# Kernel optimization log

Hardware: AMD Instinct MI355X
Metric: run time of the kernel (lower is better)

## Reference

```python
import jax, jax.numpy as jnp
import numpy as np
import math

D_MODEL = 2048
NUM_HEADS = 32
NUM_KV_HEADS = 8
HEAD_DIM = D_MODEL // NUM_HEADS  # 64
BATCH = 2
SEQ = 2048


def setup_inputs() -> dict:
    key = jax.random.key(0)
    ks = jax.random.split(key, 5)
    std_q = math.sqrt(2.0 / (D_MODEL + D_MODEL))
    std_kv = math.sqrt(2.0 / (D_MODEL + NUM_KV_HEADS * HEAD_DIM))
    x = jax.random.normal(ks[0], (BATCH, SEQ, D_MODEL), dtype=jnp.float32)
    Wq = jax.random.normal(ks[1], (D_MODEL, D_MODEL), dtype=jnp.float32) * std_q
    Wk = jax.random.normal(ks[2], (NUM_KV_HEADS * HEAD_DIM, D_MODEL), dtype=jnp.float32) * std_kv
    Wv = jax.random.normal(ks[3], (NUM_KV_HEADS * HEAD_DIM, D_MODEL), dtype=jnp.float32) * std_kv
    Wo = jax.random.normal(ks[4], (D_MODEL, D_MODEL), dtype=jnp.float32) * std_q
    return {"x": x, "Wq": Wq, "Wk": Wk, "Wv": Wv, "Wo": Wo}


def reference(x, Wq, Wk, Wv, Wo):
    B, L, _ = x.shape
    group = NUM_HEADS // NUM_KV_HEADS
    # projections: x @ W.T
    q = (x @ Wq.T).reshape(B, L, NUM_HEADS, HEAD_DIM).transpose(0, 2, 1, 3)      # [B,H,L,D]
    k = (x @ Wk.T).reshape(B, L, NUM_KV_HEADS, HEAD_DIM).transpose(0, 2, 1, 3)   # [B,Hkv,L,D]
    v = (x @ Wv.T).reshape(B, L, NUM_KV_HEADS, HEAD_DIM).transpose(0, 2, 1, 3)
    # expand KV heads (repeat_interleave along head dim)
    k = jnp.repeat(k, group, axis=1)  # [B,H,L,D]
    v = jnp.repeat(v, group, axis=1)
    scale = 1.0 / math.sqrt(HEAD_DIM)
    scores = jnp.einsum("bhld,bhsd->bhls", q, k) * scale  # [B,H,L,S]
    causal_mask = jnp.tril(jnp.ones((L, L), dtype=bool))
    scores = jnp.where(causal_mask[None, None], scores, -jnp.inf)
    weights = jax.nn.softmax(scores, axis=-1)
    out = jnp.einsum("bhls,bhsd->bhld", weights, v)  # [B,H,L,D]
    out = out.transpose(0, 2, 1, 3).reshape(B, L, D_MODEL)
    return out @ Wo.T
```

## Files before the change

### kernel.cpp

```cpp
#include <hip/hip_runtime.h>
#include <stdint.h>


typedef unsigned short u16;
typedef short bf16x8 __attribute__((ext_vector_type(8)));
typedef float f32x4 __attribute__((ext_vector_type(4)));

#define D_MODEL 2048
#define QKV_DIM 3072
#define NUM_HEADS 32
#define HEAD_DIM 64
#define SEQ 2048
#define MTOT 4096

static __device__ __forceinline__ u16 f2bf(float f){
  uint32_t u = __builtin_bit_cast(uint32_t, f);
  u += 0x7FFFu + ((u >> 16) & 1u);
  return (u16)(u >> 16);
}

static __device__ __forceinline__ float exp2_fast(float x){
  float r;
  asm("v_exp_f32 %0, %1" : "=v"(r) : "v"(x));
  return r;
}

static __device__ __forceinline__ uint32_t cvt_pk_bf16(float lo, float hi){
  uint32_t r;
  asm("v_cvt_pk_bf16_f32 %0, %1, %2" : "=v"(r) : "v"(lo), "v"(hi));
  return r;
}

static __device__ __forceinline__ void gload16(const u16* g, u16* l){
  __builtin_amdgcn_global_load_lds(
      (__attribute__((address_space(1))) uint32_t*)(uintptr_t)g,
      (__attribute__((address_space(3))) uint32_t*)l,
      16, 0, 0);
}

static __device__ __forceinline__ void cvt8(const float* __restrict__ src,
                                            u16* __restrict__ dst,
                                            int i, float scl){
  float4 a = *(const float4*)(src + i);
  float4 b = *(const float4*)(src + i + 4);
  union { u16 h[8]; uint4 v; } t;
  t.h[0]=f2bf(a.x*scl); t.h[1]=f2bf(a.y*scl); t.h[2]=f2bf(a.z*scl); t.h[3]=f2bf(a.w*scl);
  t.h[4]=f2bf(b.x*scl); t.h[5]=f2bf(b.y*scl); t.h[6]=f2bf(b.z*scl); t.h[7]=f2bf(b.w*scl);
  *(uint4*)(dst + i) = t.v;
}

__global__ __launch_bounds__(256)
void cvt_bf16(const float* __restrict__ in, u16* __restrict__ out, int n,
              float scl){
  const int i = (blockIdx.x * 256 + threadIdx.x) * 8;
  if (i >= n) return;
  cvt8(in, out, i, scl);
}

__global__ __launch_bounds__(256)
void cvt_all(const float* __restrict__ x,  const float* __restrict__ Wq,
             const float* __restrict__ Wk, const float* __restrict__ Wv,
             const float* __restrict__ Wo,
             u16* __restrict__ xb, u16* __restrict__ Wb,
             u16* __restrict__ Wob, float qscl){
  const int bid = blockIdx.x;
  const float* src; u16* dst; int off; float scl = 1.0f;
  if (bid < 4096){        src = x;  dst = xb;                              off = bid;        }
  else if (bid < 6144){   src = Wq; dst = Wb;                              off = bid - 4096; scl = qscl; }
  else if (bid < 6656){   src = Wk; dst = Wb + (size_t)D_MODEL*D_MODEL;    off = bid - 6144; }
  else if (bid < 7168){   src = Wv; dst = Wb + (size_t)2560*D_MODEL;       off = bid - 6656; }
  else {                  src = Wo; dst = Wob;                             off = bid - 7168; }
  const int i = (off * 256 + threadIdx.x) * 8;
  cvt8(src, dst, i, scl);
}

template <bool F32OUT>
__global__ __launch_bounds__(256)
void gemm_bt(const u16* __restrict__ A, const u16* __restrict__ B,
             void* __restrict__ Cv, int M, int N, int K, int nbx){
  constexpr int BK = 32;
  __shared__ __attribute__((aligned(16))) u16 As[128*BK];
  __shared__ __attribute__((aligned(16))) u16 Bs[128*BK];
  const int tid  = threadIdx.x;
  const int wave = tid >> 6, lane = tid & 63;
  const int quad = lane >> 4, l16 = lane & 15;
  const int wrow = wave >> 1, wcol = wave & 1;
  const int nwg = gridDim.x;
  const int qq = nwg >> 3, rr = nwg & 7;
  const int xcd = blockIdx.x & 7, lin = blockIdx.x >> 3;
  const int swz = (xcd < rr ? xcd*(qq+1) : rr*(qq+1) + (xcd-rr)*qq) + lin;
  const int m0 = (swz / nbx) * 128, n0 = (swz % nbx) * 128;
  const int srow = lane >> 2, scol = (lane & 3) * 8;

  const f32x4 zero = {0.f, 0.f, 0.f, 0.f};
  f32x4 acc[4][4];
#pragma unroll
  for (int i = 0; i < 4; i++)
#pragma unroll
    for (int j = 0; j < 4; j++) acc[i][j] = zero;

  for (int k0 = 0; k0 < K; k0 += BK){
#pragma unroll
    for (int t = 0; t < 2; t++){
      const int chunk = wave + t*4;
      gload16(A + (size_t)(m0 + chunk*16 + srow)*K + k0 + scol, As + chunk*16*BK);
      gload16(B + (size_t)(n0 + chunk*16 + srow)*K + k0 + scol, Bs + chunk*16*BK);
    }
    __syncthreads();
    bf16x8 af[4], bfr[4];
#pragma unroll
    for (int mi = 0; mi < 4; mi++)
      af[mi] = *(const bf16x8*)(As + (wrow*64 + mi*16 + l16)*BK + quad*8);
#pragma unroll
    for (int ni = 0; ni < 4; ni++)
      bfr[ni] = *(const bf16x8*)(Bs + (wcol*64 + ni*16 + l16)*BK + quad*8);
#pragma unroll
    for (int mi = 0; mi < 4; mi++)
#pragma unroll
      for (int ni = 0; ni < 4; ni++)
        acc[mi][ni] = __builtin_amdgcn_mfma_f32_16x16x32_bf16(af[mi], bfr[ni], acc[mi][ni], 0, 0, 0);
    __syncthreads();
  }
#pragma unroll
  for (int mi = 0; mi < 4; mi++)
#pragma unroll
    for (int ni = 0; ni < 4; ni++){
      const int col = n0 + wcol*64 + ni*16 + l16;
#pragma unroll
      for (int r = 0; r < 4; r++){
        const int row = m0 + wrow*64 + mi*16 + quad*4 + r;
        if constexpr (F32OUT)
          ((float*)Cv)[(size_t)row*N + col] = acc[mi][ni][r];
        else
          ((u16*)Cv)[(size_t)row*N + col] = f2bf(acc[mi][ni][r]);
      }
    }
}

__global__ __launch_bounds__(256)
void kvtrans(const u16* __restrict__ QKV, u16* __restrict__ Ksw,
             u16* __restrict__ Vsw){
  __shared__ u16 Ls[64*72];
  const int tid = threadIdx.x;
  const int st = blockIdx.x, hk = blockIdx.y, b = blockIdx.z;
  const size_t rb = (size_t)b * SEQ;
  const size_t tbase = ((size_t)(b*8 + hk)*32 + st) * 4096;

#pragma unroll
  for (int t = 0; t < 2; t++){
    const int task = t*256 + tid;
    const int r = task >> 3, c = task & 7;
    uint4 kv = *(const uint4*)(QKV + (rb + st*64 + r)*QKV_DIM + 2048 + hk*HEAD_DIM + c*8);
    *(uint4*)(Ksw + tbase + r*64 + (size_t)((c ^ (r & 7)) * 8)) = kv;
  }
#pragma unroll
  for (int t = 0; t < 2; t++){
    const int task = t*256 + tid;
    const int r = task >> 3, c = task & 7;
    *(uint4*)(Ls + r*72 + c*8) =
        *(const uint4*)(QKV + (rb + st*64 + r)*QKV_DIM + 2560 + hk*HEAD_DIM + c*8);
  }
  __syncthreads();
#pragma unroll
  for (int t = 0; t < 2; t++){
    const int task = t*256 + tid;
    const int d = task >> 3, sc = task & 7;
    union { u16 h[8]; uint4 v; } tmp;
#pragma unroll
    for (int e = 0; e < 8; e++){
      const int key = ((2*(sc>>2) + (e>>2))<<4) + ((sc&3)<<2) + (e&3);
      tmp.h[e] = Ls[key*72 + d];
    }
    *(uint4*)(Vsw + tbase + d*64 + (size_t)((sc ^ (d & 7)) * 8)) = tmp.v;
  }
}

__global__ __launch_bounds__(256)
void attn(const u16* __restrict__ Q, const u16* __restrict__ Ksw,
          const u16* __restrict__ Vsw, u16* __restrict__ O, int qs){
  __shared__ __attribute__((aligned(16))) u16 Ks[2][64*64];
  __shared__ __attribute__((aligned(16))) u16 Vt[2][64*64];
  const int tid = threadIdx.x;
  const int wave = tid >> 6, lane = tid & 63, quad = lane >> 4, l16 = lane & 15;
  const int g_ = (blockIdx.x + blockIdx.y) & 31;
  const int qt = blockIdx.z ? (31 - g_) : g_;
  const int h = blockIdx.y, b = blockIdx.z;
  const int hk = h >> 2;
  const size_t rb = (size_t)b * SEQ;
  const size_t hb = ((size_t)(b*8 + hk)) * 32;

  const int qrow = wave*16 + l16;
  const int sw = l16 & 7;

  bf16x8 qf[2];
  {
    const u16* qp = Q + (rb + qt*64 + wave*16 + l16)*qs + h*HEAD_DIM;
    qf[0] = *(const bf16x8*)(qp + quad*8);
    qf[1] = *(const bf16x8*)(qp + 32 + quad*8);
  }
  const f32x4 zero = {0.f, 0.f, 0.f, 0.f};
  f32x4 oacc[4];
#pragma unroll
  for (int i = 0; i < 4; i++) oacc[i] = zero;
  float m_i = -INFINITY;
  float l_i = 0.f;

  {
    const u16* kt = Ksw + hb * 4096;
    const u16* vt = Vsw + hb * 4096;
#pragma unroll
    for (int t = 0; t < 2; t++){
      const int ch = wave*2 + t;
      gload16(kt + ch*512 + lane*8, &Ks[0][ch*512]);
      gload16(vt + ch*512 + lane*8, &Vt[0][ch*512]);
    }
  }
  int cur = 0;

  for (int j = 0; j <= qt; ++j){
    __syncthreads();
    if (j < qt){
      const u16* kt = Ksw + (hb + j + 1) * 4096;
      const u16* vt = Vsw + (hb + j + 1) * 4096;
#pragma unroll
      for (int t = 0; t < 2; t++){
        const int ch = wave*2 + t;
        gload16(kt + ch*512 + lane*8, &Ks[cur^1][ch*512]);
        gload16(vt + ch*512 + lane*8, &Vt[cur^1][ch*512]);
      }
    }
    const u16* Ksb = Ks[cur];
    const u16* Vtb = Vt[cur];

    f32x4 st[4];
#pragma unroll
    for (int ni = 0; ni < 4; ni++){
      f32x4 s = zero;
#pragma unroll
      for (int ss = 0; ss < 2; ss++){
        bf16x8 kf = *(const bf16x8*)(Ksb + ((ni*16 + l16) << 6) +
                                     (((ss*4 + quad) ^ sw) << 3));
        s = __builtin_amdgcn_mfma_f32_16x16x32_bf16(kf, qf[ss], s, 0, 0, 0);
      }
      st[ni] = s;
    }
    if (j == qt){
#pragma unroll
      for (int ni = 0; ni < 4; ni++)
#pragma unroll
        for (int r = 0; r < 4; r++)
          if (ni*16 + quad*4 + r > qrow) st[ni][r] = -INFINITY;
    }

    float mx = fmaxf(fmaxf(fmaxf(st[0][0], st[0][1]), fmaxf(st[0][2], st[0][3])),
                     fmaxf(fmaxf(st[1][0], st[1][1]), fmaxf(st[1][2], st[1][3])));
    mx = fmaxf(mx, fmaxf(fmaxf(fmaxf(st[2][0], st[2][1]), fmaxf(st[2][2], st[2][3])),
                         fmaxf(fmaxf(st[3][0], st[3][1]), fmaxf(st[3][2], st[3][3]))));
    mx = fmaxf(mx, __shfl_xor(mx, 16));
    mx = fmaxf(mx, __shfl_xor(mx, 32));

    if (__all(mx <= m_i + 10.f)){
      float ps = 0.f;
#pragma unroll
      for (int ni = 0; ni < 4; ni++)
#pragma unroll
        for (int r = 0; r < 4; r++){
          const float p = exp2_fast(st[ni][r] - m_i);
          st[ni][r] = p;
          ps += p;
        }
      ps += __shfl_xor(ps, 16);
      ps += __shfl_xor(ps, 32);
      l_i += ps;
    } else {
      const float mn = fmaxf(m_i, mx);
      const float alpha = exp2_fast(m_i - mn);
      float ps = 0.f;
#pragma unroll
      for (int ni = 0; ni < 4; ni++)
#pragma unroll
        for (int r = 0; r < 4; r++){
          const float p = exp2_fast(st[ni][r] - mn);
          st[ni][r] = p;
          ps += p;
        }
      ps += __shfl_xor(ps, 16);
      ps += __shfl_xor(ps, 32);
      l_i = l_i*alpha + ps;
      m_i = mn;
      float ar[4];
#pragma unroll
      for (int r = 0; r < 4; r++) ar[r] = __shfl(alpha, quad*4 + r);
#pragma unroll
      for (int ci = 0; ci < 4; ci++)
#pragma unroll
        for (int r = 0; r < 4; r++) oacc[ci][r] *= ar[r];
    }

    bf16x8 pfr[2];
#pragma unroll
    for (int ss = 0; ss < 2; ss++){
      union { uint32_t w[4]; bf16x8 v; } pk;
      pk.w[0] = cvt_pk_bf16(st[2*ss][0],   st[2*ss][1]);
      pk.w[1] = cvt_pk_bf16(st[2*ss][2],   st[2*ss][3]);
      pk.w[2] = cvt_pk_bf16(st[2*ss+1][0], st[2*ss+1][1]);
      pk.w[3] = cvt_pk_bf16(st[2*ss+1][2], st[2*ss+1][3]);
      pfr[ss] = pk.v;
    }

#pragma unroll
    for (int ss = 0; ss < 2; ss++)
#pragma unroll
      for (int ci = 0; ci < 4; ci++){
        bf16x8 vf = *(const bf16x8*)(Vtb + ((ci*16 + l16) << 6) +
                                     (((ss*4 + quad) ^ sw) << 3));
        oacc[ci] = __builtin_amdgcn_mfma_f32_16x16x32_bf16(pfr[ss], vf, oacc[ci], 0, 0, 0);
      }
    cur ^= 1;
  }

  float lf[4];
#pragma unroll
  for (int r = 0; r < 4; r++) lf[r] = __shfl(l_i, quad*4 + r);
#pragma unroll
  for (int ci = 0; ci < 4; ci++)
#pragma unroll
    for (int r = 0; r < 4; r++){
      const size_t row = rb + qt*64 + wave*16 + quad*4 + r;
      O[row*D_MODEL + h*HEAD_DIM + ci*16 + l16] = f2bf(oacc[ci][r] / lf[r]);
    }
}

extern "C" void kernel_launch(void* const* d_in, const int* in_sizes, int n_in,
                              void* d_out, int out_size, void* d_ws, size_t ws_size,
                              hipStream_t stream){
  const float* x  = (const float*)d_in[0];
  const float* Wq = (const float*)d_in[1];
  const float* Wk = (const float*)d_in[2];
  const float* Wv = (const float*)d_in[3];
  const float* Wo = (const float*)d_in[4];
  float* out = (float*)d_out;

  u16* xb   = (u16*)d_ws;
  u16* Wb   = xb + (size_t)MTOT*D_MODEL;
  u16* Wob  = Wb + (size_t)QKV_DIM*D_MODEL;
  u16* QKVb = (u16*)d_out;
  u16* Kswz = Wb;
  u16* Vswz = Wb + (size_t)2*1024*1024;

  const int nwq = D_MODEL*D_MODEL;
  const float QSCL = 0.125f * 1.44269504f;

  const size_t ws_need = ((size_t)MTOT*D_MODEL + (size_t)QKV_DIM*D_MODEL +
                          (size_t)D_MODEL*D_MODEL) * sizeof(u16);
  const bool wob_fits = (ws_size >= ws_need);

  if (wob_fits){
    cvt_all<<<9216, 256, 0, stream>>>(x, Wq, Wk, Wv, Wo, xb, Wb, Wob, QSCL);
  } else {
    cvt_all<<<7168, 256, 0, stream>>>(x, Wq, Wk, Wv, Wo, xb, Wb, Wob, QSCL);
  }
  gemm_bt<false><<<(QKV_DIM/128)*(MTOT/128), 256, 0, stream>>>(
      xb, Wb, QKVb, MTOT, QKV_DIM, D_MODEL, QKV_DIM/128);
  kvtrans<<<dim3(SEQ/64, 8, 2), 256, 0, stream>>>(QKVb, Kswz, Vswz);
  attn<<<dim3(SEQ/64, NUM_HEADS, 2), 256, 0, stream>>>(
      QKVb, Kswz, Vswz, xb, QKV_DIM);
  const u16* Bw2;
  if (wob_fits){
    Bw2 = Wob;
  } else {
    cvt_bf16<<<nwq/2048, 256, 0, stream>>>(Wo, Wb, nwq, 1.0f);
    Bw2 = Wb;
  }
  gemm_bt<true><<<(D_MODEL/128)*(MTOT/128), 256, 0, stream>>>(
      xb, Bw2, (void*)out, MTOT, D_MODEL, D_MODEL, D_MODEL/128);
}
```

Baseline: 326.3 us.

## Replace 128x128 GEMM with double-buffered 256x256 tile GEMM using swizzled LDS

Replaces the projection GEMMs with a 256x256-tile, 512-thread kernel that uses BK=64 and double-buffered LDS. Loads for the next stages are issued before they are needed, with waits controlled by vmcnt. An XOR swizzle on the LDS layout is meant to avoid bank conflicts, and raised wave priority is used around the MFMA bursts. The aim is more operand reuse per global load and hiding of load latency behind compute. In exchange it uses 128KB of LDS and many more accumulator registers, and launches far fewer workgroups (192 and 128), which may underfill the 256 CUs.

Result: no change. 331.4 us (+1.6%).

```diff
diff --git a/kernel.cpp b/kernel.cpp
--- a/kernel.cpp
+++ b/kernel.cpp
@@ -75,64 +75,102 @@
 }
 
 template <bool F32OUT>
-__global__ __launch_bounds__(256)
-void gemm_bt(const u16* __restrict__ A, const u16* __restrict__ B,
+__global__ __launch_bounds__(512)
+void gemm256(const u16* __restrict__ A, const u16* __restrict__ B,
              void* __restrict__ Cv, int M, int N, int K, int nbx){
-  constexpr int BK = 32;
-  __shared__ __attribute__((aligned(16))) u16 As[128*BK];
-  __shared__ __attribute__((aligned(16))) u16 Bs[128*BK];
-  const int tid  = threadIdx.x;
-  const int wave = tid >> 6, lane = tid & 63;
+  __shared__ __attribute__((aligned(16))) u16 As[2][256*64];
+  __shared__ __attribute__((aligned(16))) u16 Bs[2][256*64];
+  const int tid = threadIdx.x;
+  const int wid = tid >> 6, lane = tid & 63;
   const int quad = lane >> 4, l16 = lane & 15;
-  const int wrow = wave >> 1, wcol = wave & 1;
+  const int wr = wid >> 2, wc = wid & 3;
+  const int sw8 = l16 & 7;
   const int nwg = gridDim.x;
   const int qq = nwg >> 3, rr = nwg & 7;
   const int xcd = blockIdx.x & 7, lin = blockIdx.x >> 3;
   const int swz = (xcd < rr ? xcd*(qq+1) : rr*(qq+1) + (xcd-rr)*qq) + lin;
-  const int m0 = (swz / nbx) * 128, n0 = (swz % nbx) * 128;
-  const int srow = lane >> 2, scol = (lane & 3) * 8;
+  const int m0 = (swz / nbx) * 256, n0 = (swz % nbx) * 256;
 
   const f32x4 zero = {0.f, 0.f, 0.f, 0.f};
-  f32x4 acc[4][4];
-#pragma unroll
-  for (int i = 0; i < 4; i++)
+  f32x4 acc[8][4];
+#pragma unroll
+  for (int i = 0; i < 8; i++)
 #pragma unroll
     for (int j = 0; j < 4; j++) acc[i][j] = zero;
 
-  for (int k0 = 0; k0 < K; k0 += BK){
-#pragma unroll
-    for (int t = 0; t < 2; t++){
-      const int chunk = wave + t*4;
-      gload16(A + (size_t)(m0 + chunk*16 + srow)*K + k0 + scol, As + chunk*16*BK);
-      gload16(B + (size_t)(n0 + chunk*16 + srow)*K + k0 + scol, Bs + chunk*16*BK);
-    }
-    __syncthreads();
-    bf16x8 af[4], bfr[4];
-#pragma unroll
-    for (int mi = 0; mi < 4; mi++)
-      af[mi] = *(const bf16x8*)(As + (wrow*64 + mi*16 + l16)*BK + quad*8);
-#pragma unroll
-    for (int ni = 0; ni < 4; ni++)
-      bfr[ni] = *(const bf16x8*)(Bs + (wcol*64 + ni*16 + l16)*BK + quad*8);
-#pragma unroll
-    for (int mi = 0; mi < 4; mi++)
-#pragma unroll
-      for (int ni = 0; ni < 4; ni++)
-        acc[mi][ni] = __builtin_amdgcn_mfma_f32_16x16x32_bf16(af[mi], bfr[ni], acc[mi][ni], 0, 0, 0);
-    __syncthreads();
-  }
-#pragma unroll
-  for (int mi = 0; mi < 4; mi++)
-#pragma unroll
-    for (int ni = 0; ni < 4; ni++){
-      const int col = n0 + wcol*64 + ni*16 + l16;
-#pragma unroll
-      for (int r = 0; r < 4; r++){
-        const int row = m0 + wrow*64 + mi*16 + quad*4 + r;
+  const int NT = K >> 6;
+
+#define STAGE(kt_, c_)                                                      \
+  {                                                                         \
+    const int k0_ = (kt_) << 6;                                             \
+    _Pragma("unroll")                                                       \
+    for (int t = 0; t < 4; ++t){                                            \
+      const int L = t*512 + tid;                                            \
+      const int r_ = L >> 3, c8_ = L & 7;                                   \
+      gload16(A + (size_t)(m0 + r_)*K + k0_ + ((c8_ ^ (r_ & 7)) << 3),      \
+              (u16*)&As[c_][(t*512 + wid*64) * 8]);                         \
+      gload16(B + (size_t)(n0 + r_)*K + k0_ + ((c8_ ^ (r_ & 7)) << 3),      \
+              (u16*)&Bs[c_][(t*512 + wid*64) * 8]);                         \
+    }                                                                       \
+  }
+
+  STAGE(0, 0);
+  STAGE(1, 1);
+
+  for (int kt = 0; kt < NT; ++kt){
+    const int c = kt & 1;
+    if (kt < NT - 1) asm volatile("s_waitcnt vmcnt(8)" ::: "memory");
+    else             asm volatile("s_waitcnt vmcnt(0)" ::: "memory");
+    __builtin_amdgcn_s_barrier();
+    __builtin_amdgcn_sched_barrier(0);
+
+    const u16* Ab = As[c];
+    const u16* Bb = Bs[c];
+    bf16x8 bfr[4][2];
+#pragma unroll
+    for (int n = 0; n < 4; ++n)
+#pragma unroll
+      for (int kk = 0; kk < 2; ++kk)
+        bfr[n][kk] = *(const bf16x8*)(Bb + (wc*64 + n*16 + l16)*64 +
+                                      (((kk*4 + quad) ^ sw8) << 3));
+#pragma unroll
+    for (int p = 0; p < 4; ++p){
+      bf16x8 af[2][2];
+#pragma unroll
+      for (int mm = 0; mm < 2; ++mm)
+#pragma unroll
+        for (int kk = 0; kk < 2; ++kk)
+          af[mm][kk] = *(const bf16x8*)(Ab + (wr*128 + (p*2+mm)*16 + l16)*64 +
+                                        (((kk*4 + quad) ^ sw8) << 3));
+      __builtin_amdgcn_s_setprio(1);
+#pragma unroll
+      for (int mm = 0; mm < 2; ++mm)
+#pragma unroll
+        for (int n = 0; n < 4; ++n)
+#pragma unroll
+          for (int kk = 0; kk < 2; ++kk)
+            acc[p*2+mm][n] = __builtin_amdgcn_mfma_f32_16x16x32_bf16(
+                af[mm][kk], bfr[n][kk], acc[p*2+mm][n], 0, 0, 0);
+      __builtin_amdgcn_s_setprio(0);
+    }
+    __builtin_amdgcn_sched_barrier(0);
+    __builtin_amdgcn_s_barrier();
+    if (kt + 2 < NT) STAGE(kt + 2, c);
+  }
+#undef STAGE
+
+#pragma unroll
+  for (int mf = 0; mf < 8; ++mf)
+#pragma unroll
+    for (int n = 0; n < 4; ++n){
+      const int col = n0 + wc*64 + n*16 + l16;
+#pragma unroll
+      for (int r = 0; r < 4; ++r){
+        const int row = m0 + wr*128 + mf*16 + quad*4 + r;
         if constexpr (F32OUT)
-          ((float*)Cv)[(size_t)row*N + col] = acc[mi][ni][r];
+          ((float*)Cv)[(size_t)row*N + col] = acc[mf][n][r];
         else
-          ((u16*)Cv)[(size_t)row*N + col] = f2bf(acc[mi][ni][r]);
+          ((u16*)Cv)[(size_t)row*N + col] = f2bf(acc[mf][n][r]);
       }
     }
 }
@@ -360,8 +398,8 @@
   } else {
     cvt_all<<<7168, 256, 0, stream>>>(x, Wq, Wk, Wv, Wo, xb, Wb, Wob, QSCL);
   }
-  gemm_bt<false><<<(QKV_DIM/128)*(MTOT/128), 256, 0, stream>>>(
-      xb, Wb, QKVb, MTOT, QKV_DIM, D_MODEL, QKV_DIM/128);
+  gemm256<false><<<(QKV_DIM/256)*(MTOT/256), 512, 0, stream>>>(
+      xb, Wb, QKVb, MTOT, QKV_DIM, D_MODEL, QKV_DIM/256);
   kvtrans<<<dim3(SEQ/64, 8, 2), 256, 0, stream>>>(QKVb, Kswz, Vswz);
   attn<<<dim3(SEQ/64, NUM_HEADS, 2), 256, 0, stream>>>(
       QKVb, Kswz, Vswz, xb, QKV_DIM);
@@ -372,6 +410,6 @@
     cvt_bf16<<<nwq/2048, 256, 0, stream>>>(Wo, Wb, nwq, 1.0f);
     Bw2 = Wb;
   }
-  gemm_bt<true><<<(D_MODEL/128)*(MTOT/128), 256, 0, stream>>>(
-      xb, Bw2, (void*)out, MTOT, D_MODEL, D_MODEL, D_MODEL/128);
-}
+  gemm256<true><<<(D_MODEL/256)*(MTOT/256), 512, 0, stream>>>(
+      xb, Bw2, (void*)out, MTOT, D_MODEL, D_MODEL, D_MODEL/256);
+}
```

## Process two KV tiles per barrier and raise wave priority around MFMAs

Applied to the files above, without the earlier changes.

The attention loop now stages two 64-key K/V tiles per double-buffer slot, which halves the number of __syncthreads barriers and issues larger prefetch batches. The per-tile work moves into a helper, and s_setprio calls bracket the QK and PV MFMA sections so matrix work gets scheduling priority over softmax from other waves. Shared memory per block doubles to 64KB, which may lower occupancy.

After: 363.1 us. 1.11x slower.

```diff
diff --git a/kernel.cpp b/kernel.cpp
--- a/kernel.cpp
+++ b/kernel.cpp
@@ -175,11 +175,104 @@
   }
 }
 
+static __device__ __forceinline__ void tile_step(
+    const u16* __restrict__ Ksb, const u16* __restrict__ Vtb,
+    const bf16x8* qf, f32x4* oacc, float& m_i, float& l_i,
+    int quad, int l16, int sw, bool diag, int qrow){
+  const f32x4 zero = {0.f, 0.f, 0.f, 0.f};
+  f32x4 st[4];
+  __builtin_amdgcn_s_setprio(1);
+#pragma unroll
+  for (int ni = 0; ni < 4; ni++){
+    f32x4 s = zero;
+#pragma unroll
+    for (int ss = 0; ss < 2; ss++){
+      bf16x8 kf = *(const bf16x8*)(Ksb + ((ni*16 + l16) << 6) +
+                                   (((ss*4 + quad) ^ sw) << 3));
+      s = __builtin_amdgcn_mfma_f32_16x16x32_bf16(kf, qf[ss], s, 0, 0, 0);
+    }
+    st[ni] = s;
+  }
+  __builtin_amdgcn_s_setprio(0);
+  if (diag){
+#pragma unroll
+    for (int ni = 0; ni < 4; ni++)
+#pragma unroll
+      for (int r = 0; r < 4; r++)
+        if (ni*16 + quad*4 + r > qrow) st[ni][r] = -INFINITY;
+  }
+  float mx = fmaxf(fmaxf(fmaxf(st[0][0], st[0][1]), fmaxf(st[0][2], st[0][3])),
+                   fmaxf(fmaxf(st[1][0], st[1][1]), fmaxf(st[1][2], st[1][3])));
+  mx = fmaxf(mx, fmaxf(fmaxf(fmaxf(st[2][0], st[2][1]), fmaxf(st[2][2], st[2][3])),
+                       fmaxf(fmaxf(st[3][0], st[3][1]), fmaxf(st[3][2], st[3][3]))));
+  mx = fmaxf(mx, __shfl_xor(mx, 16));
+  mx = fmaxf(mx, __shfl_xor(mx, 32));
+
+  if (__all(mx <= m_i + 10.f)){
+    float ps = 0.f;
+#pragma unroll
+    for (int ni = 0; ni < 4; ni++)
+#pragma unroll
+      for (int r = 0; r < 4; r++){
+        const float p = exp2_fast(st[ni][r] - m_i);
+        st[ni][r] = p;
+        ps += p;
+      }
+    ps += __shfl_xor(ps, 16);
+    ps += __shfl_xor(ps, 32);
+    l_i += ps;
+  } else {
+    const float mn = fmaxf(m_i, mx);
+    const float alpha = exp2_fast(m_i - mn);
+    float ps = 0.f;
+#pragma unroll
+    for (int ni = 0; ni < 4; ni++)
+#pragma unroll
+      for (int r = 0; r < 4; r++){
+        const float p = exp2_fast(st[ni][r] - mn);
+        st[ni][r] = p;
+        ps += p;
+      }
+    ps += __shfl_xor(ps, 16);
+    ps += __shfl_xor(ps, 32);
+    l_i = l_i*alpha + ps;
+    m_i = mn;
+    float ar[4];
+#pragma unroll
+    for (int r = 0; r < 4; r++) ar[r] = __shfl(alpha, quad*4 + r);
+#pragma unroll
+    for (int ci = 0; ci < 4; ci++)
+#pragma unroll
+      for (int r = 0; r < 4; r++) oacc[ci][r] *= ar[r];
+  }
+
+  bf16x8 pfr[2];
+#pragma unroll
+  for (int ss = 0; ss < 2; ss++){
+    union { uint32_t w[4]; bf16x8 v; } pk;
+    pk.w[0] = cvt_pk_bf16(st[2*ss][0],   st[2*ss][1]);
+    pk.w[1] = cvt_pk_bf16(st[2*ss][2],   st[2*ss][3]);
+    pk.w[2] = cvt_pk_bf16(st[2*ss+1][0], st[2*ss+1][1]);
+    pk.w[3] = cvt_pk_bf16(st[2*ss+1][2], st[2*ss+1][3]);
+    pfr[ss] = pk.v;
+  }
+  __builtin_amdgcn_s_setprio(1);
+#pragma unroll
+  for (int ss = 0; ss < 2; ss++)
+#pragma unroll
+    for (int ci = 0; ci < 4; ci++){
+      bf16x8 vf = *(const bf16x8*)(Vtb + ((ci*16 + l16) << 6) +
+                                   (((ss*4 + quad) ^ sw) << 3));
+      oacc[ci] = __builtin_amdgcn_mfma_f32_16x16x32_bf16(pfr[ss], vf, oacc[ci], 0, 0, 0);
+    }
+  __builtin_amdgcn_s_setprio(0);
+}
+
 __global__ __launch_bounds__(256)
 void attn(const u16* __restrict__ Q, const u16* __restrict__ Ksw,
           const u16* __restrict__ Vsw, u16* __restrict__ O, int qs){
-  __shared__ __attribute__((aligned(16))) u16 Ks[2][64*64];
-  __shared__ __attribute__((aligned(16))) u16 Vt[2][64*64];
+  __shared__ __attribute__((aligned(16))) u16 Ks[2][2*4096];
+  __shared__ __attribute__((aligned(16))) u16 Vt[2][2*4096];
   const int tid = threadIdx.x;
   const int wave = tid >> 6, lane = tid & 63, quad = lane >> 4, l16 = lane & 15;
   const int g_ = (blockIdx.x + blockIdx.y) & 31;
@@ -205,119 +298,40 @@
   float m_i = -INFINITY;
   float l_i = 0.f;
 
-  {
-    const u16* kt = Ksw + hb * 4096;
-    const u16* vt = Vsw + hb * 4096;
-#pragma unroll
-    for (int t = 0; t < 2; t++){
-      const int ch = wave*2 + t;
-      gload16(kt + ch*512 + lane*8, &Ks[0][ch*512]);
-      gload16(vt + ch*512 + lane*8, &Vt[0][ch*512]);
-    }
-  }
+#define STAGE_T(j_, buf_, slot_)                                            \
+  {                                                                         \
+    const u16* kt_ = Ksw + (hb + (j_)) * 4096;                              \
+    const u16* vt_ = Vsw + (hb + (j_)) * 4096;                              \
+    _Pragma("unroll")                                                       \
+    for (int t = 0; t < 2; t++){                                            \
+      const int ch = wave*2 + t;                                            \
+      gload16(kt_ + ch*512 + lane*8, &Ks[buf_][(slot_)*4096 + ch*512]);     \
+      gload16(vt_ + ch*512 + lane*8, &Vt[buf_][(slot_)*4096 + ch*512]);     \
+    }                                                                       \
+  }
+
+  const int NP = (qt >> 1) + 1;
+
+  STAGE_T(0, 0, 0);
+  if (qt >= 1) STAGE_T(1, 0, 1);
   int cur = 0;
 
-  for (int j = 0; j <= qt; ++j){
+  for (int p = 0; p < NP; ++p){
     __syncthreads();
-    if (j < qt){
-      const u16* kt = Ksw + (hb + j + 1) * 4096;
-      const u16* vt = Vsw + (hb + j + 1) * 4096;
-#pragma unroll
-      for (int t = 0; t < 2; t++){
-        const int ch = wave*2 + t;
-        gload16(kt + ch*512 + lane*8, &Ks[cur^1][ch*512]);
-        gload16(vt + ch*512 + lane*8, &Vt[cur^1][ch*512]);
-      }
-    }
-    const u16* Ksb = Ks[cur];
-    const u16* Vtb = Vt[cur];
-
-    f32x4 st[4];
-#pragma unroll
-    for (int ni = 0; ni < 4; ni++){
-      f32x4 s = zero;
-#pragma unroll
-      for (int ss = 0; ss < 2; ss++){
-        bf16x8 kf = *(const bf16x8*)(Ksb + ((ni*16 + l16) << 6) +
-                                     (((ss*4 + quad) ^ sw) << 3));
-        s = __builtin_amdgcn_mfma_f32_16x16x32_bf16(kf, qf[ss], s, 0, 0, 0);
-      }
-      st[ni] = s;
-    }
-    if (j == qt){
-#pragma unroll
-      for (int ni = 0; ni < 4; ni++)
-#pragma unroll
-        for (int r = 0; r < 4; r++)
-          if (ni*16 + quad*4 + r > qrow) st[ni][r] = -INFINITY;
-    }
-
-    float mx = fmaxf(fmaxf(fmaxf(st[0][0], st[0][1]), fmaxf(st[0][2], st[0][3])),
-                     fmaxf(fmaxf(st[1][0], st[1][1]), fmaxf(st[1][2], st[1][3])));
-    mx = fmaxf(mx, fmaxf(fmaxf(fmaxf(st[2][0], st[2][1]), fmaxf(st[2][2], st[2][3])),
-                         fmaxf(fmaxf(st[3][0], st[3][1]), fmaxf(st[3][2], st[3][3]))));
-    mx = fmaxf(mx, __shfl_xor(mx, 16));
-    mx = fmaxf(mx, __shfl_xor(mx, 32));
-
-    if (__all(mx <= m_i + 10.f)){
-      float ps = 0.f;
-#pragma unroll
-      for (int ni = 0; ni < 4; ni++)
-#pragma unroll
-        for (int r = 0; r < 4; r++){
-          const float p = exp2_fast(st[ni][r] - m_i);
-          st[ni][r] = p;
-          ps += p;
-        }
-      ps += __shfl_xor(ps, 16);
-      ps += __shfl_xor(ps, 32);
-      l_i += ps;
-    } else {
-      const float mn = fmaxf(m_i, mx);
-      const float alpha = exp2_fast(m_i - mn);
-      float ps = 0.f;
-#pragma unroll
-      for (int ni = 0; ni < 4; ni++)
-#pragma unroll
-        for (int r = 0; r < 4; r++){
-          const float p = exp2_fast(st[ni][r] - mn);
-          st[ni][r] = p;
-          ps += p;
-        }
-      ps += __shfl_xor(ps, 16);
-      ps += __shfl_xor(ps, 32);
-      l_i = l_i*alpha + ps;
-      m_i = mn;
-      float ar[4];
-#pragma unroll
-      for (int r = 0; r < 4; r++) ar[r] = __shfl(alpha, quad*4 + r);
-#pragma unroll
-      for (int ci = 0; ci < 4; ci++)
-#pragma unroll
-        for (int r = 0; r < 4; r++) oacc[ci][r] *= ar[r];
-    }
-
-    bf16x8 pfr[2];
-#pragma unroll
-    for (int ss = 0; ss < 2; ss++){
-      union { uint32_t w[4]; bf16x8 v; } pk;
-      pk.w[0] = cvt_pk_bf16(st[2*ss][0],   st[2*ss][1]);
-      pk.w[1] = cvt_pk_bf16(st[2*ss][2],   st[2*ss][3]);
-      pk.w[2] = cvt_pk_bf16(st[2*ss+1][0], st[2*ss+1][1]);
-      pk.w[3] = cvt_pk_bf16(st[2*ss+1][2], st[2*ss+1][3]);
-      pfr[ss] = pk.v;
-    }
-
-#pragma unroll
-    for (int ss = 0; ss < 2; ss++)
-#pragma unroll
-      for (int ci = 0; ci < 4; ci++){
-        bf16x8 vf = *(const bf16x8*)(Vtb + ((ci*16 + l16) << 6) +
-                                     (((ss*4 + quad) ^ sw) << 3));
-        oacc[ci] = __builtin_amdgcn_mfma_f32_16x16x32_bf16(pfr[ss], vf, oacc[ci], 0, 0, 0);
-      }
+    if (p + 1 < NP){
+      const int jn = 2*p + 2;
+      STAGE_T(jn, cur^1, 0);
+      if (jn + 1 <= qt) STAGE_T(jn + 1, cur^1, 1);
+    }
+    const int j0 = 2*p;
+    tile_step(&Ks[cur][0], &Vt[cur][0], qf, oacc, m_i, l_i,
+              quad, l16, sw, j0 == qt, qrow);
+    if (j0 + 1 <= qt)
+      tile_step(&Ks[cur][4096], &Vt[cur][4096], qf, oacc, m_i, l_i,
+                quad, l16, sw, j0 + 1 == qt, qrow);
     cur ^= 1;
   }
+#undef STAGE_T
 
   float lf[4];
 #pragma unroll
```

## Process 128 query rows per attention block with 8 waves sharing KV tiles

Applied to the files above, without the earlier changes.

The attention kernel now launches 512-thread blocks covering 128 query rows (two 64-row tiles) instead of 256-thread blocks covering 64 rows. Each KV tile staged in shared memory is reused by twice as many waves, which halves KV global-to-LDS traffic per query row. Waves in the first half skip the final KV tile, where their rows are fully masked, and apply the causal mask at their own diagonal. The trade-off is half as many blocks, with the lower waves idle on the last iteration, and a heavier register and occupancy footprint per block.

Result: no change. 321.6 us (-1.5%).

```diff
diff --git a/kernel.cpp b/kernel.cpp
--- a/kernel.cpp
+++ b/kernel.cpp
@@ -175,26 +175,28 @@
   }
 }
 
-__global__ __launch_bounds__(256)
+__global__ __launch_bounds__(512)
 void attn(const u16* __restrict__ Q, const u16* __restrict__ Ksw,
           const u16* __restrict__ Vsw, u16* __restrict__ O, int qs){
-  __shared__ __attribute__((aligned(16))) u16 Ks[2][64*64];
-  __shared__ __attribute__((aligned(16))) u16 Vt[2][64*64];
+  __shared__ __attribute__((aligned(16))) u16 Ks[2][4096];
+  __shared__ __attribute__((aligned(16))) u16 Vt[2][4096];
   const int tid = threadIdx.x;
-  const int wave = tid >> 6, lane = tid & 63, quad = lane >> 4, l16 = lane & 15;
-  const int g_ = (blockIdx.x + blockIdx.y) & 31;
-  const int qt = blockIdx.z ? (31 - g_) : g_;
+  const int wid = tid >> 6, lane = tid & 63, quad = lane >> 4, l16 = lane & 15;
+  const int g_ = (blockIdx.x + blockIdx.y) & 15;
+  const int tb = blockIdx.z ? (15 - g_) : g_;
   const int h = blockIdx.y, b = blockIdx.z;
   const int hk = h >> 2;
   const size_t rb = (size_t)b * SEQ;
   const size_t hb = ((size_t)(b*8 + hk)) * 32;
 
-  const int qrow = wave*16 + l16;
+  const int qtB   = 2*tb + 1;
+  const int jmaxw = 2*tb + (wid >> 2);
+  const int qrow  = (wid & 3)*16 + l16;
   const int sw = l16 & 7;
 
   bf16x8 qf[2];
   {
-    const u16* qp = Q + (rb + qt*64 + wave*16 + l16)*qs + h*HEAD_DIM;
+    const u16* qp = Q + (rb + tb*128 + wid*16 + l16)*qs + h*HEAD_DIM;
     qf[0] = *(const bf16x8*)(qp + quad*8);
     qf[1] = *(const bf16x8*)(qp + 32 + quad*8);
   }
@@ -205,119 +207,111 @@
   float m_i = -INFINITY;
   float l_i = 0.f;
 
-  {
-    const u16* kt = Ksw + hb * 4096;
-    const u16* vt = Vsw + hb * 4096;
-#pragma unroll
-    for (int t = 0; t < 2; t++){
-      const int ch = wave*2 + t;
-      gload16(kt + ch*512 + lane*8, &Ks[0][ch*512]);
-      gload16(vt + ch*512 + lane*8, &Vt[0][ch*512]);
-    }
-  }
+#define STAGE_T(j_, buf_)                                                   \
+  {                                                                         \
+    gload16(Ksw + (hb + (j_)) * 4096 + wid*512 + lane*8, &Ks[buf_][wid*512]); \
+    gload16(Vsw + (hb + (j_)) * 4096 + wid*512 + lane*8, &Vt[buf_][wid*512]); \
+  }
+
+  STAGE_T(0, 0);
   int cur = 0;
 
-  for (int j = 0; j <= qt; ++j){
+  for (int j = 0; j <= qtB; ++j){
     __syncthreads();
-    if (j < qt){
-      const u16* kt = Ksw + (hb + j + 1) * 4096;
-      const u16* vt = Vsw + (hb + j + 1) * 4096;
-#pragma unroll
-      for (int t = 0; t < 2; t++){
-        const int ch = wave*2 + t;
-        gload16(kt + ch*512 + lane*8, &Ks[cur^1][ch*512]);
-        gload16(vt + ch*512 + lane*8, &Vt[cur^1][ch*512]);
-      }
-    }
-    const u16* Ksb = Ks[cur];
-    const u16* Vtb = Vt[cur];
-
-    f32x4 st[4];
-#pragma unroll
-    for (int ni = 0; ni < 4; ni++){
-      f32x4 s = zero;
+    if (j < qtB) STAGE_T(j + 1, cur^1);
+
+    if (j <= jmaxw){
+      const u16* Ksb = Ks[cur];
+      const u16* Vtb = Vt[cur];
+
+      f32x4 st[4];
+#pragma unroll
+      for (int ni = 0; ni < 4; ni++){
+        f32x4 s = zero;
+#pragma unroll
+        for (int ss = 0; ss < 2; ss++){
+          bf16x8 kf = *(const bf16x8*)(Ksb + ((ni*16 + l16) << 6) +
+                                       (((ss*4 + quad) ^ sw) << 3));
+          s = __builtin_amdgcn_mfma_f32_16x16x32_bf16(kf, qf[ss], s, 0, 0, 0);
+        }
+        st[ni] = s;
+      }
+      if (j == jmaxw){
+#pragma unroll
+        for (int ni = 0; ni < 4; ni++)
+#pragma unroll
+          for (int r = 0; r < 4; r++)
+            if (ni*16 + quad*4 + r > qrow) st[ni][r] = -INFINITY;
+      }
+
+      float mx = fmaxf(fmaxf(fmaxf(st[0][0], st[0][1]), fmaxf(st[0][2], st[0][3])),
+                       fmaxf(fmaxf(st[1][0], st[1][1]), fmaxf(st[1][2], st[1][3])));
+      mx = fmaxf(mx, fmaxf(fmaxf(fmaxf(st[2][0], st[2][1]), fmaxf(st[2][2], st[2][3])),
+                           fmaxf(fmaxf(st[3][0], st[3][1]), fmaxf(st[3][2], st[3][3]))));
+      mx = fmaxf(mx, __shfl_xor(mx, 16));
+      mx = fmaxf(mx, __shfl_xor(mx, 32));
+
+      if (__all(mx <= m_i + 10.f)){
+        float ps = 0.f;
+#pragma unroll
+        for (int ni = 0; ni < 4; ni++)
+#pragma unroll
+          for (int r = 0; r < 4; r++){
+            const float p = exp2_fast(st[ni][r] - m_i);
+            st[ni][r] = p;
+            ps += p;
+          }
+        ps += __shfl_xor(ps, 16);
+        ps += __shfl_xor(ps, 32);
+        l_i += ps;
+      } else {
+        const float mn = fmaxf(m_i, mx);
+        const float alpha = exp2_fast(m_i - mn);
+        float ps = 0.f;
+#pragma unroll
+        for (int ni = 0; ni < 4; ni++)
+#pragma unroll
+          for (int r = 0; r < 4; r++){
+            const float p = exp2_fast(st[ni][r] - mn);
+            st[ni][r] = p;
+            ps += p;
+          }
+        ps += __shfl_xor(ps, 16);
+        ps += __shfl_xor(ps, 32);
+        l_i = l_i*alpha + ps;
+        m_i = mn;
+        float ar[4];
+#pragma unroll
+        for (int r = 0; r < 4; r++) ar[r] = __shfl(alpha, quad*4 + r);
+#pragma unroll
+        for (int ci = 0; ci < 4; ci++)
+#pragma unroll
+          for (int r = 0; r < 4; r++) oacc[ci][r] *= ar[r];
+      }
+
+      bf16x8 pfr[2];
 #pragma unroll
       for (int ss = 0; ss < 2; ss++){
-        bf16x8 kf = *(const bf16x8*)(Ksb + ((ni*16 + l16) << 6) +
-                                     (((ss*4 + quad) ^ sw) << 3));
-        s = __builtin_amdgcn_mfma_f32_16x16x32_bf16(kf, qf[ss], s, 0, 0, 0);
-      }
-      st[ni] = s;
-    }
-    if (j == qt){
-#pragma unroll
-      for (int ni = 0; ni < 4; ni++)
-#pragma unroll
-        for (int r = 0; r < 4; r++)
-          if (ni*16 + quad*4 + r > qrow) st[ni][r] = -INFINITY;
-    }
-
-    float mx = fmaxf(fmaxf(fmaxf(st[0][0], st[0][1]), fmaxf(st[0][2], st[0][3])),
-                     fmaxf(fmaxf(st[1][0], st[1][1]), fmaxf(st[1][2], st[1][3])));
-    mx = fmaxf(mx, fmaxf(fmaxf(fmaxf(st[2][0], st[2][1]), fmaxf(st[2][2], st[2][3])),
-                         fmaxf(fmaxf(st[3][0], st[3][1]), fmaxf(st[3][2], st[3][3]))));
-    mx = fmaxf(mx, __shfl_xor(mx, 16));
-    mx = fmaxf(mx, __shfl_xor(mx, 32));
-
-    if (__all(mx <= m_i + 10.f)){
-      float ps = 0.f;
-#pragma unroll
-      for (int ni = 0; ni < 4; ni++)
-#pragma unroll
-        for (int r = 0; r < 4; r++){
-          const float p = exp2_fast(st[ni][r] - m_i);
-          st[ni][r] = p;
-          ps += p;
+        union { uint32_t w[4]; bf16x8 v; } pk;
+        pk.w[0] = cvt_pk_bf16(st[2*ss][0],   st[2*ss][1]);
+        pk.w[1] = cvt_pk_bf16(st[2*ss][2],   st[2*ss][3]);
+        pk.w[2] = cvt_pk_bf16(st[2*ss+1][0], st[2*ss+1][1]);
+        pk.w[3] = cvt_pk_bf16(st[2*ss+1][2], st[2*ss+1][3]);
+        pfr[ss] = pk.v;
+      }
+
+#pragma unroll
+      for (int ss = 0; ss < 2; ss++)
+#pragma unroll
+        for (int ci = 0; ci < 4; ci++){
+          bf16x8 vf = *(const bf16x8*)(Vtb + ((ci*16 + l16) << 6) +
+                                       (((ss*4 + quad) ^ sw) << 3));
+          oacc[ci] = __builtin_amdgcn_mfma_f32_16x16x32_bf16(pfr[ss], vf, oacc[ci], 0, 0, 0);
         }
-      ps += __shfl_xor(ps, 16);
-      ps += __shfl_xor(ps, 32);
-      l_i += ps;
-    } else {
-      const float mn = fmaxf(m_i, mx);
-      const float alpha = exp2_fast(m_i - mn);
-      float ps = 0.f;
-#pragma unroll
-      for (int ni = 0; ni < 4; ni++)
-#pragma unroll
-        for (int r = 0; r < 4; r++){
-          const float p = exp2_fast(st[ni][r] - mn);
-          st[ni][r] = p;
-          ps += p;
-        }
-      ps += __shfl_xor(ps, 16);
-      ps += __shfl_xor(ps, 32);
-      l_i = l_i*alpha + ps;
-      m_i = mn;
-      float ar[4];
-#pragma unroll
-      for (int r = 0; r < 4; r++) ar[r] = __shfl(alpha, quad*4 + r);
-#pragma unroll
-      for (int ci = 0; ci < 4; ci++)
-#pragma unroll
-        for (int r = 0; r < 4; r++) oacc[ci][r] *= ar[r];
-    }
-
-    bf16x8 pfr[2];
-#pragma unroll
-    for (int ss = 0; ss < 2; ss++){
-      union { uint32_t w[4]; bf16x8 v; } pk;
-      pk.w[0] = cvt_pk_bf16(st[2*ss][0],   st[2*ss][1]);
-      pk.w[1] = cvt_pk_bf16(st[2*ss][2],   st[2*ss][3]);
-      pk.w[2] = cvt_pk_bf16(st[2*ss+1][0], st[2*ss+1][1]);
-      pk.w[3] = cvt_pk_bf16(st[2*ss+1][2], st[2*ss+1][3]);
-      pfr[ss] = pk.v;
-    }
-
-#pragma unroll
-    for (int ss = 0; ss < 2; ss++)
-#pragma unroll
-      for (int ci = 0; ci < 4; ci++){
-        bf16x8 vf = *(const bf16x8*)(Vtb + ((ci*16 + l16) << 6) +
-                                     (((ss*4 + quad) ^ sw) << 3));
-        oacc[ci] = __builtin_amdgcn_mfma_f32_16x16x32_bf16(pfr[ss], vf, oacc[ci], 0, 0, 0);
-      }
+    }
     cur ^= 1;
   }
+#undef STAGE_T
 
   float lf[4];
 #pragma unroll
@@ -326,7 +320,7 @@
   for (int ci = 0; ci < 4; ci++)
 #pragma unroll
     for (int r = 0; r < 4; r++){
-      const size_t row = rb + qt*64 + wave*16 + quad*4 + r;
+      const size_t row = rb + tb*128 + wid*16 + quad*4 + r;
       O[row*D_MODEL + h*HEAD_DIM + ci*16 + l16] = f2bf(oacc[ci][r] / lf[r]);
     }
 }
@@ -363,7 +357,7 @@
   gemm_bt<false><<<(QKV_DIM/128)*(MTOT/128), 256, 0, stream>>>(
       xb, Wb, QKVb, MTOT, QKV_DIM, D_MODEL, QKV_DIM/128);
   kvtrans<<<dim3(SEQ/64, 8, 2), 256, 0, stream>>>(QKVb, Kswz, Vswz);
-  attn<<<dim3(SEQ/64, NUM_HEADS, 2), 256, 0, stream>>>(
+  attn<<<dim3(16, NUM_HEADS, 2), 512, 0, stream>>>(
       QKVb, Kswz, Vswz, xb, QKV_DIM);
   const u16* Bw2;
   if (wob_fits){
```
